# Kernel optimization log

Hardware: AMD Instinct MI355X
Metric: run time of the kernel (lower is better)

The kernel has to match this reference:

```python
import jax, jax.numpy as jnp
import numpy as np


def setup_inputs() -> dict:
    key = jax.random.key(0)
    ks = jax.random.split(key, 9)
    B, L, D, H, E = 8, 2048, 1024, 256, 8
    Hg = D // 4
    s = 0.02
    return {
        "x": jax.random.normal(ks[0], (B, L, D), dtype=jnp.float32),
        "wg1": jax.random.normal(ks[1], (D, Hg), dtype=jnp.float32) * s,
        "bg1": jax.random.normal(ks[2], (Hg,), dtype=jnp.float32) * s,
        "wg2": jax.random.normal(ks[3], (Hg, E), dtype=jnp.float32) * s,
        "bg2": jax.random.normal(ks[4], (E,), dtype=jnp.float32) * s,
        "w1": jax.random.normal(ks[5], (E, D, H), dtype=jnp.float32) * (1.0 / np.sqrt(D)),
        "b1": jax.random.normal(ks[6], (E, H), dtype=jnp.float32) * s,
        "w2": jax.random.normal(ks[7], (E, H, D), dtype=jnp.float32) * (1.0 / np.sqrt(H)),
        "b2": jax.random.normal(ks[8], (E, D), dtype=jnp.float32) * s,
        "k": 2,
    }


def reference(x, wg1, bg1, wg2, bg2, w1, b1, w2, b2, k):
    B, L, D = x.shape
    xt = x.reshape(-1, D)                       # [T, D] tokens
    T = xt.shape[0]
    # gating MLP: Linear -> GELU(exact, matches torch nn.GELU) -> Linear -> softmax
    logits = jax.nn.gelu(xt @ wg1 + bg1, approximate=False) @ wg2 + bg2  # [T, E]
    scores = jax.nn.softmax(logits, axis=-1)
    top_v, top_i = jax.lax.top_k(scores, k)     # [T, k]
    # dense gate matrix (equivalent to compute_gating's scatter); zeros for non-top-k
    gates = jnp.zeros_like(scores).at[jnp.arange(T)[:, None], top_i].set(top_v)  # [T, E]

    # grouped-GEMM MoE: y[t] = sum_e gates[t,e] * (gelu(x[t] @ W1_e + b1_e) @ W2_e + b2_e)
    # scan over the fixed, small expert axis; gates zero out non-selected experts,
    # giving math identical to the sort/dispatch + per-expert torch.mm loop.
    def body(acc, we):
        w1e, b1e, w2e, b2e, ge = we
        h = jax.nn.gelu(xt @ w1e + b1e, approximate=False)  # [T, H]
        o = h @ w2e + b2e                                    # [T, D]
        return acc + ge[:, None] * o, None

    y, _ = jax.lax.scan(body, jnp.zeros_like(xt), (w1, b1, w2, b2, gates.T))
    return y.reshape(B, L, D)
```

## Files before the change

### kernel.cpp

```cpp
#include <hip/hip_runtime.h>

typedef unsigned short u16;
typedef __attribute__((ext_vector_type(8))) short bf16x8;
typedef __attribute__((ext_vector_type(4))) float f32x4;
typedef __attribute__((ext_vector_type(4))) u16 u16x4;

#define T_TOK 16384
#define D_DIM 1024
#define NE 8
#define MAXP 33792

__device__ __forceinline__ u16 f2bf(float f) {
  union { float f; unsigned int u; } c; c.f = f;
  unsigned int u = c.u;
  u += 0x7fffu + ((u >> 16) & 1u);
  return (u16)(u >> 16);
}

__device__ __forceinline__ float bf2f(u16 v) {
  union { unsigned int u; float f; } c; c.u = ((unsigned int)v) << 16;
  return c.f;
}

__device__ __forceinline__ float gelu_exact(float u) {
  return 0.5f * u * (1.0f + erff(u * 0.70710678118654752f));
}

__device__ __forceinline__ void gld16(const void* g, void* l) {
  __builtin_amdgcn_global_load_lds(
      (const __attribute__((address_space(1))) unsigned int*)g,
      (__attribute__((address_space(3))) unsigned int*)l, 16, 0, 0);
}

__device__ __forceinline__ void stage_tile(u16* lds, const char* g0, size_t stride,
                                           int wid, int lane) {
  const char* g = g0 + (size_t)(wid * 8 + (lane >> 3)) * stride + (size_t)((lane & 7) * 16);
  char* l = (char*)lds + wid * 1024;
  #pragma unroll
  for (int c = 0; c < 4; ++c)
    gld16(g + (size_t)(32 * c) * stride, l + c * 4096);
}

__device__ __forceinline__ void stage_b32(u16* lds, const u16* mat, int rowbase,
                                          int k0, int wid, int lane) {
  const char* g0 = (const char*)(mat + (size_t)rowbase * 1024 + k0);
  #pragma unroll
  for (int c = 0; c < 2; ++c) {
    const int row = c * 64 + wid * 16 + (lane >> 2);
    const char* g = g0 + (size_t)row * 2048 + (size_t)((lane & 3) * 16);
    char* l = (char*)lds + c * 4096 + wid * 1024;
    gld16(g, l);
  }
}

__device__ __forceinline__ void mma_step(const u16* As, const u16* Bs, f32x4 acc[4][4],
                                         int wm, int wn, int lane) {
  const int r = lane & 15, kq = (lane >> 4) * 8;
  #pragma unroll
  for (int ks = 0; ks < 2; ++ks) {
    const int col = ks * 32 + kq;
    bf16x8 a[4], b[4];
    #pragma unroll
    for (int mf = 0; mf < 4; ++mf)
      a[mf] = *(const bf16x8*)&As[(wm * 64 + mf * 16 + r) * 64 + col];
    #pragma unroll
    for (int nf = 0; nf < 4; ++nf)
      b[nf] = *(const bf16x8*)&Bs[(wn * 64 + nf * 16 + r) * 64 + col];
    #pragma unroll
    for (int mf = 0; mf < 4; ++mf)
      #pragma unroll
      for (int nf = 0; nf < 4; ++nf)
        acc[mf][nf] = __builtin_amdgcn_mfma_f32_16x16x32_bf16(a[mf], b[nf], acc[mf][nf], 0, 0, 0);
  }
}

__global__ __launch_bounds__(256) void transpose_cvt_kernel(const float* __restrict__ in,
                                                            u16* __restrict__ out,
                                                            int R, int C) {
  __shared__ u16 t[32][36];
  const int e = blockIdx.z;
  const int r0 = blockIdx.x * 32, c0 = blockIdx.y * 32;
  const int tid = threadIdx.x;
  {
    const int r = tid >> 3, cq = (tid & 7) * 4;
    float4 v = *(const float4*)(in + ((size_t)e * R + r0 + r) * C + c0 + cq);
    t[r][cq + 0] = f2bf(v.x); t[r][cq + 1] = f2bf(v.y);
    t[r][cq + 2] = f2bf(v.z); t[r][cq + 3] = f2bf(v.w);
  }
  __syncthreads();
  {
    const int c = tid >> 3, rq = (tid & 7) * 4;
    u16x4 o;
    o.x = t[rq + 0][c]; o.y = t[rq + 1][c]; o.z = t[rq + 2][c]; o.w = t[rq + 3][c];
    *(u16x4*)(out + ((size_t)e * C + c0 + c) * R + r0 + rq) = o;
  }
}

__global__ __launch_bounds__(256) void transpose_hilo_kernel(const float* __restrict__ in,
                                                             u16* __restrict__ out_hi,
                                                             u16* __restrict__ out_lo,
                                                             int R, int C) {
  __shared__ u16 th[32][36];
  __shared__ u16 tl[32][36];
  const int r0 = blockIdx.x * 32, c0 = blockIdx.y * 32;
  const int tid = threadIdx.x;
  {
    const int r = tid >> 3, cq = (tid & 7) * 4;
    float4 v = *(const float4*)(in + (size_t)(r0 + r) * C + c0 + cq);
    float vv[4] = {v.x, v.y, v.z, v.w};
    #pragma unroll
    for (int i = 0; i < 4; ++i) {
      u16 h = f2bf(vv[i]);
      th[r][cq + i] = h;
      tl[r][cq + i] = f2bf(vv[i] - bf2f(h));
    }
  }
  __syncthreads();
  {
    const int c = tid >> 3, rq = (tid & 7) * 4;
    u16x4 oh, ol;
    oh.x = th[rq + 0][c]; oh.y = th[rq + 1][c]; oh.z = th[rq + 2][c]; oh.w = th[rq + 3][c];
    ol.x = tl[rq + 0][c]; ol.y = tl[rq + 1][c]; ol.z = tl[rq + 2][c]; ol.w = tl[rq + 3][c];
    *(u16x4*)(out_hi + (size_t)(c0 + c) * R + r0 + rq) = oh;
    *(u16x4*)(out_lo + (size_t)(c0 + c) * R + r0 + rq) = ol;
  }
}

__global__ __launch_bounds__(256) void gating_mfma_kernel(
    const float* __restrict__ x, const u16* __restrict__ wg1t_hi,
    const u16* __restrict__ wg1t_lo, u16* __restrict__ xb,
    float* __restrict__ p_buf) {
  __shared__ u16 Ah[2][128 * 32], Al[2][128 * 32];
  __shared__ u16 Bh[2][128 * 32], Bl[2][128 * 32];
  const int tid = threadIdx.x, lane = tid & 63, wid = tid >> 6;
  const int t0 = blockIdx.x * 128, n0 = blockIdx.y * 128;
  const int kh = blockIdx.z, kbeg = kh * 512;
  const int wm = wid >> 1, wn = wid & 1;
  const bool emit = (blockIdx.y == 0);
  const int arow = tid >> 1, akb = (tid & 1) * 16;

  f32x4 acc[4][4];
  #pragma unroll
  for (int i = 0; i < 4; ++i)
    #pragma unroll
    for (int j = 0; j < 4; ++j) acc[i][j] = (f32x4){0.f, 0.f, 0.f, 0.f};

  stage_b32(Bh[0], wg1t_hi, n0, kbeg, wid, lane);
  stage_b32(Bl[0], wg1t_lo, n0, kbeg, wid, lane);
  {
    const float* src = x + (size_t)(t0 + arow) * 1024 + kbeg + akb;
    #pragma unroll
    for (int i = 0; i < 4; ++i) {
      float4 v = *(const float4*)(src + i * 4);
      float vv[4] = {v.x, v.y, v.z, v.w};
      u16x4 h, l;
      u16 hh[4], ll[4];
      #pragma unroll
      for (int q = 0; q < 4; ++q) { hh[q] = f2bf(vv[q]); ll[q] = f2bf(vv[q] - bf2f(hh[q])); }
      h.x = hh[0]; h.y = hh[1]; h.z = hh[2]; h.w = hh[3];
      l.x = ll[0]; l.y = ll[1]; l.z = ll[2]; l.w = ll[3];
      *(u16x4*)&Ah[0][arow * 32 + akb + i * 4] = h;
      *(u16x4*)&Al[0][arow * 32 + akb + i * 4] = l;
      if (emit) *(u16x4*)(xb + (size_t)(t0 + arow) * 1024 + kbeg + akb + i * 4) = h;
    }
  }
  __syncthreads();

  int cur = 0;
  for (int kt = 0; kt < 16; ++kt) {
    const bool has_next = kt < 15;
    const int nxt = cur ^ 1;
    float4 xv[4];
    if (has_next) {
      stage_b32(Bh[nxt], wg1t_hi, n0, kbeg + (kt + 1) * 32, wid, lane);
      stage_b32(Bl[nxt], wg1t_lo, n0, kbeg + (kt + 1) * 32, wid, lane);
      const float* src = x + (size_t)(t0 + arow) * 1024 + kbeg + (kt + 1) * 32 + akb;
      #pragma unroll
      for (int i = 0; i < 4; ++i) xv[i] = *(const float4*)(src + i * 4);
    }
    {
      const int r = lane & 15, kq = (lane >> 4) * 8;
      bf16x8 ah[4], al[4], bh[4], bl[4];
      #pragma unroll
      for (int mf = 0; mf < 4; ++mf) {
        const int ro = (wm * 64 + mf * 16 + r) * 32 + kq;
        ah[mf] = *(const bf16x8*)&Ah[cur][ro];
        al[mf] = *(const bf16x8*)&Al[cur][ro];
      }
      #pragma unroll
      for (int nf = 0; nf < 4; ++nf) {
        const int ro = (wn * 64 + nf * 16 + r) * 32 + kq;
        bh[nf] = *(const bf16x8*)&Bh[cur][ro];
        bl[nf] = *(const bf16x8*)&Bl[cur][ro];
      }
      #pragma unroll
      for (int mf = 0; mf < 4; ++mf)
        #pragma unroll
        for (int nf = 0; nf < 4; ++nf) {
          acc[mf][nf] = __builtin_amdgcn_mfma_f32_16x16x32_bf16(ah[mf], bh[nf], acc[mf][nf], 0, 0, 0);
          acc[mf][nf] = __builtin_amdgcn_mfma_f32_16x16x32_bf16(ah[mf], bl[nf], acc[mf][nf], 0, 0, 0);
          acc[mf][nf] = __builtin_amdgcn_mfma_f32_16x16x32_bf16(al[mf], bh[nf], acc[mf][nf], 0, 0, 0);
        }
    }
    if (has_next) {
      #pragma unroll
      for (int i = 0; i < 4; ++i) {
        float vv[4] = {xv[i].x, xv[i].y, xv[i].z, xv[i].w};
        u16x4 h, l;
        u16 hh[4], ll[4];
        #pragma unroll
        for (int q = 0; q < 4; ++q) { hh[q] = f2bf(vv[q]); ll[q] = f2bf(vv[q] - bf2f(hh[q])); }
        h.x = hh[0]; h.y = hh[1]; h.z = hh[2]; h.w = hh[3];
        l.x = ll[0]; l.y = ll[1]; l.z = ll[2]; l.w = ll[3];
        *(u16x4*)&Ah[nxt][arow * 32 + akb + i * 4] = h;
        *(u16x4*)&Al[nxt][arow * 32 + akb + i * 4] = l;
        if (emit)
          *(u16x4*)(xb + (size_t)(t0 + arow) * 1024 + kbeg + (kt + 1) * 32 + akb + i * 4) = h;
      }
    }
    __syncthreads();
    cur ^= 1;
  }

  #pragma unroll
  for (int mf = 0; mf < 4; ++mf)
    #pragma unroll
    for (int rr = 0; rr < 4; ++rr) {
      const int lt = wm * 64 + mf * 16 + ((lane >> 4) << 2) + rr;
      #pragma unroll
      for (int nf = 0; nf < 4; ++nf) {
        const int ln = wn * 64 + nf * 16 + (lane & 15);
        p_buf[((size_t)kh * T_TOK + t0 + lt) * 256 + n0 + ln] = acc[mf][nf][rr];
      }
    }
}

__global__ __launch_bounds__(256) void gating_p2_kernel(
    const float* __restrict__ p_buf, const float* __restrict__ bg1,
    const float* __restrict__ wg2, const float* __restrict__ bg2,
    int* __restrict__ top_i, float2* __restrict__ top_g) {
  const int tid = threadIdx.x;
  const int tn = tid & 31, tm = tid >> 5;
  const int t0 = blockIdx.x * 32;

  float bb[8];
  {
    float4 ba = *(const float4*)&bg1[tn * 4];
    float4 bc = *(const float4*)&bg1[128 + tn * 4];
    bb[0] = ba.x; bb[1] = ba.y; bb[2] = ba.z; bb[3] = ba.w;
    bb[4] = bc.x; bb[5] = bc.y; bb[6] = bc.z; bb[7] = bc.w;
  }

  float hv[4][8];
  #pragma unroll
  for (int i = 0; i < 4; ++i) {
    const size_t t = t0 + tm * 4 + i;
    const float* pa = &p_buf[t * 256];
    const float* pb = &p_buf[((size_t)T_TOK + t) * 256];
    float4 a0 = *(const float4*)&pa[tn * 4];
    float4 a1 = *(const float4*)&pa[128 + tn * 4];
    float4 b0 = *(const float4*)&pb[tn * 4];
    float4 b1 = *(const float4*)&pb[128 + tn * 4];
    hv[i][0] = gelu_exact(a0.x + b0.x + bb[0]);
    hv[i][1] = gelu_exact(a0.y + b0.y + bb[1]);
    hv[i][2] = gelu_exact(a0.z + b0.z + bb[2]);
    hv[i][3] = gelu_exact(a0.w + b0.w + bb[3]);
    hv[i][4] = gelu_exact(a1.x + b1.x + bb[4]);
    hv[i][5] = gelu_exact(a1.y + b1.y + bb[5]);
    hv[i][6] = gelu_exact(a1.z + b1.z + bb[6]);
    hv[i][7] = gelu_exact(a1.w + b1.w + bb[7]);
  }

  float part[4][8];
  #pragma unroll
  for (int i = 0; i < 4; ++i)
    #pragma unroll
    for (int e = 0; e < 8; ++e) part[i][e] = 0.f;
  #pragma unroll
  for (int j = 0; j < 8; ++j) {
    const int col = (j < 4) ? (tn * 4 + j) : (128 + tn * 4 + (j - 4));
    float4 wa = *(const float4*)&wg2[col * 8];
    float4 wb = *(const float4*)&wg2[col * 8 + 4];
    float we[8] = {wa.x, wa.y, wa.z, wa.w, wb.x, wb.y, wb.z, wb.w};
    #pragma unroll
    for (int i = 0; i < 4; ++i)
      #pragma unroll
      for (int e = 0; e < 8; ++e) part[i][e] += hv[i][j] * we[e];
  }
  #pragma unroll
  for (int mask = 1; mask < 32; mask <<= 1)
    #pragma unroll
    for (int i = 0; i < 4; ++i)
      #pragma unroll
      for (int e = 0; e < 8; ++e) part[i][e] += __shfl_xor(part[i][e], mask);

  if (tn < 4) {
    float lg[8];
    #pragma unroll
    for (int i = 0; i < 4; ++i)
      if (tn == i) {
        #pragma unroll
        for (int e = 0; e < 8; ++e) lg[e] = part[i][e];
      }
    #pragma unroll
    for (int e = 0; e < 8; ++e) lg[e] += bg2[e];
    float m = lg[0];
    #pragma unroll
    for (int e = 1; e < 8; ++e) m = fmaxf(m, lg[e]);
    float ex[8], s = 0.f;
    #pragma unroll
    for (int e = 0; e < 8; ++e) { ex[e] = expf(lg[e] - m); s += ex[e]; }
    int i1 = 0;
    #pragma unroll
    for (int e = 1; e < 8; ++e) if (lg[e] > lg[i1]) i1 = e;
    int i2 = (i1 == 0) ? 1 : 0;
    #pragma unroll
    for (int e = 0; e < 8; ++e) if (e != i1 && lg[e] > lg[i2]) i2 = e;
    float inv = 1.f / s;
    const int t = t0 + tm * 4 + tn;
    top_i[t] = i1 | (i2 << 8);
    top_g[t] = make_float2(ex[i1] * inv, ex[i2] * inv);
  }
}

__global__ __launch_bounds__(256) void hist_kernel(const int* __restrict__ top_i,
                                                   int* __restrict__ hist) {
  __shared__ int h[NE];
  const int tid = threadIdx.x;
  if (tid < NE) h[tid] = 0;
  __syncthreads();
  const int ti = top_i[blockIdx.x * 256 + tid];
  atomicAdd(&h[ti & 255], 1);
  atomicAdd(&h[ti >> 8], 1);
  __syncthreads();
  if (tid < NE) hist[blockIdx.x * NE + tid] = h[tid];
}

__global__ __launch_bounds__(64) void scan_kernel(const int* __restrict__ hist,
                                                  int* __restrict__ cnt,
                                                  int* __restrict__ offs,
                                                  int* __restrict__ cbase) {
  __shared__ int tot[NE], off_s[NE];
  const int tid = threadIdx.x;
  if (tid < NE) {
    int s = 0;
    for (int c = 0; c < 64; ++c) s += hist[c * NE + tid];
    tot[tid] = s; cnt[tid] = s;
  }
  __syncthreads();
  if (tid == 0) {
    int o = 0;
    #pragma unroll
    for (int e = 0; e < NE; ++e) { off_s[e] = o; o += (tot[e] + 127) & ~127; }
  }
  __syncthreads();
  if (tid < NE) {
    offs[tid] = off_s[tid];
    int r = off_s[tid];
    for (int c = 0; c < 64; ++c) { cbase[c * NE + tid] = r; r += hist[c * NE + tid]; }
  }
}

__global__ __launch_bounds__(256) void fill_kernel(
    const int* __restrict__ top_i, const int* __restrict__ cbase,
    int* __restrict__ tok_list, int* __restrict__ pos1, int* __restrict__ pos2) {
  __shared__ int lcnt[NE];
  const int tid = threadIdx.x;
  if (tid < NE) lcnt[tid] = 0;
  __syncthreads();
  const int t = blockIdx.x * 256 + tid;
  const int ti = top_i[t];
  const int i1 = ti & 255, i2 = ti >> 8;
  const int r1 = atomicAdd(&lcnt[i1], 1);
  const int r2 = atomicAdd(&lcnt[i2], 1);
  const int p1 = cbase[blockIdx.x * NE + i1] + r1;
  const int p2 = cbase[blockIdx.x * NE + i2] + r2;
  tok_list[p1] = t; tok_list[p2] = t;
  pos1[t] = p1; pos2[t] = p2;
}

__global__ __launch_bounds__(256) void expert_h_kernel(
    const u16* __restrict__ xb, const u16* __restrict__ w1t,
    const float* __restrict__ b1, const int* __restrict__ tok_list,
    const int* __restrict__ cnt, const int* __restrict__ offs,
    u16* __restrict__ h_c) {
  __shared__ u16 As[64 * 64];
  __shared__ u16 Bs[128 * 64];
  __shared__ float b1_s[128];
  const int e = blockIdx.z;
  const int nblk = (cnt[e] + 63) >> 6;
  if ((int)blockIdx.x >= nblk) return;
  const int tid = threadIdx.x, lane = tid & 63, wid = tid >> 6;
  const int base = offs[e] + blockIdx.x * 64;
  const int n0 = blockIdx.y * 128;
  const int wm = wid >> 1, wn = wid & 1;

  if (tid < 128) b1_s[tid] = b1[e * 256 + n0 + tid];

  int tk[2];
  #pragma unroll
  for (int c = 0; c < 2; ++c)
    tk[c] = tok_list[base + (wid * 2 + c) * 8 + (lane >> 3)];

  f32x4 acc[2][4];
  #pragma unroll
  for (int i = 0; i < 2; ++i)
    #pragma unroll
    for (int j = 0; j < 4; ++j) acc[i][j] = (f32x4){0.f, 0.f, 0.f, 0.f};

  const char* Bb = (const char*)w1t + ((size_t)e * 256 + n0) * 2048;
  const int cb = (lane & 7) * 16;
  for (int kt = 0; kt < 16; ++kt) {
    __syncthreads();
    {
      char* l = (char*)As + wid * 2048;
      #pragma unroll
      for (int c = 0; c < 2; ++c)
        gld16((const char*)xb + (size_t)tk[c] * 2048 + kt * 128 + cb, l + c * 1024);
    }
    stage_tile(Bs, Bb + kt * 128, 2048, wid, lane);
    __syncthreads();
    {
      const int r = lane & 15, kq = (lane >> 4) * 8;
      #pragma unroll
      for (int ks = 0; ks < 2; ++ks) {
        const int col = ks * 32 + kq;
        bf16x8 a[2], b[4];
        #pragma unroll
        for (int mf = 0; mf < 2; ++mf)
          a[mf] = *(const bf16x8*)&As[(wm * 32 + mf * 16 + r) * 64 + col];
        #pragma unroll
        for (int nf = 0; nf < 4; ++nf)
          b[nf] = *(const bf16x8*)&Bs[(wn * 64 + nf * 16 + r) * 64 + col];
        #pragma unroll
        for (int mf = 0; mf < 2; ++mf)
          #pragma unroll
          for (int nf = 0; nf < 4; ++nf)
            acc[mf][nf] = __builtin_amdgcn_mfma_f32_16x16x32_bf16(a[mf], b[nf], acc[mf][nf], 0, 0, 0);
      }
    }
  }

  #pragma unroll
  for (int mf = 0; mf < 2; ++mf)
    #pragma unroll
    for (int rr = 0; rr < 4; ++rr) {
      const int lt = wm * 32 + mf * 16 + ((lane >> 4) << 2) + rr;
      #pragma unroll
      for (int nf = 0; nf < 4; ++nf) {
        const int ln = wn * 64 + nf * 16 + (lane & 15);
        float u = acc[mf][nf][rr] + b1_s[ln];
        h_c[(size_t)(base + lt) * 256 + n0 + ln] = f2bf(gelu_exact(u));
      }
    }
}

__global__ __launch_bounds__(256) void moe_out_kernel(
    const u16* __restrict__ h_c, const u16* __restrict__ w2t,
    const float* __restrict__ b2, const int* __restrict__ cnt,
    const int* __restrict__ offs, u16* __restrict__ o_c) {
  __shared__ u16 As[128 * 64];
  __shared__ u16 Bs[128 * 64];
  __shared__ float b2_s[128];
  const int e = blockIdx.z;
  const int nblk = (cnt[e] + 127) >> 7;
  if ((int)blockIdx.x >= nblk) return;
  const int tid = threadIdx.x, lane = tid & 63, wid = tid >> 6;
  const int base = offs[e] + blockIdx.x * 128;
  const int n0 = blockIdx.y * 128;
  const int wm = wid >> 1, wn = wid & 1;

  if (tid < 128) b2_s[tid] = b2[(size_t)e * 1024 + n0 + tid];

  f32x4 acc[4][4];
  #pragma unroll
  for (int i = 0; i < 4; ++i)
    #pragma unroll
    for (int j = 0; j < 4; ++j) acc[i][j] = (f32x4){0.f, 0.f, 0.f, 0.f};

  const char* Ab = (const char*)h_c + (size_t)base * 512;
  const char* Bb = (const char*)w2t + ((size_t)e * D_DIM + n0) * 512;
  #pragma unroll 1
  for (int kt = 0; kt < 4; ++kt) {
    __syncthreads();
    stage_tile(As, Ab + kt * 128, 512, wid, lane);
    stage_tile(Bs, Bb + kt * 128, 512, wid, lane);
    __syncthreads();
    mma_step(As, Bs, acc, wm, wn, lane);
  }

  #pragma unroll
  for (int mf = 0; mf < 4; ++mf)
    #pragma unroll
    for (int rr = 0; rr < 4; ++rr) {
      const int lt = wm * 64 + mf * 16 + ((lane >> 4) << 2) + rr;
      #pragma unroll
      for (int nf = 0; nf < 4; ++nf) {
        const int ln = wn * 64 + nf * 16 + (lane & 15);
        o_c[(size_t)(base + lt) * 1024 + n0 + ln] = f2bf(acc[mf][nf][rr] + b2_s[ln]);
      }
    }
}

__global__ __launch_bounds__(256) void gather_kernel(
    const u16* __restrict__ o_c, const int* __restrict__ pos1,
    const int* __restrict__ pos2, const float2* __restrict__ top_g,
    float* __restrict__ y) {
  const int t = blockIdx.x;
  const int p1 = pos1[t], p2 = pos2[t];
  const float2 g = top_g[t];
  const int c = threadIdx.x * 4;
  u16x4 a = *(const u16x4*)&o_c[(size_t)p1 * 1024 + c];
  u16x4 b = *(const u16x4*)&o_c[(size_t)p2 * 1024 + c];
  float4 o;
  o.x = g.x * bf2f(a.x) + g.y * bf2f(b.x);
  o.y = g.x * bf2f(a.y) + g.y * bf2f(b.y);
  o.z = g.x * bf2f(a.z) + g.y * bf2f(b.z);
  o.w = g.x * bf2f(a.w) + g.y * bf2f(b.w);
  *(float4*)&y[(size_t)t * 1024 + c] = o;
}

extern "C" void kernel_launch(void* const* d_in, const int* in_sizes, int n_in,
                              void* d_out, int out_size, void* d_ws, size_t ws_size,
                              hipStream_t stream) {
  (void)in_sizes; (void)n_in; (void)out_size; (void)ws_size;
  const float* x   = (const float*)d_in[0];
  const float* wg1 = (const float*)d_in[1];
  const float* bg1 = (const float*)d_in[2];
  const float* wg2 = (const float*)d_in[3];
  const float* bg2 = (const float*)d_in[4];
  const float* w1  = (const float*)d_in[5];
  const float* b1  = (const float*)d_in[6];
  const float* w2  = (const float*)d_in[7];
  const float* b2  = (const float*)d_in[8];
  float* y = (float*)d_out;

  char* ws = (char*)d_ws;
  u16* xb   = (u16*)(ws);
  u16* w1t  = (u16*)(ws + 33554432);
  u16* w2t  = (u16*)(ws + 37748736);
  char* M   = ws + 41943040;
  int*    cnt      = (int*)(M);
  int*    offs     = (int*)(M + 64);
  int*    hist     = (int*)(M + 128);
  int*    cbase    = (int*)(M + 2304);
  int*    tok_list = (int*)(M + 4608);
  int*    top_i    = (int*)(M + 139776);
  float2* top_g    = (float2*)(M + 205312);
  int*    pos1     = (int*)(M + 336384);
  int*    pos2     = (int*)(M + 401920);
  u16* h_c = (u16*)(ws + 42467328);
  u16* o_c = (u16*)(ws + 59768832);
  float* p_buf   = (float*)(ws + 59768832);
  u16*   wg1t_hi = (u16*)(ws + 93323264);
  u16*   wg1t_lo = (u16*)(ws + 93847552);

  hipMemsetAsync(tok_list, 0, 135168, stream);
  transpose_cvt_kernel<<<dim3(32, 8, 8), 256, 0, stream>>>(w1, w1t, 1024, 256);
  transpose_cvt_kernel<<<dim3(8, 32, 8), 256, 0, stream>>>(w2, w2t, 256, 1024);
  transpose_hilo_kernel<<<dim3(32, 8), 256, 0, stream>>>(wg1, wg1t_hi, wg1t_lo, 1024, 256);
  gating_mfma_kernel<<<dim3(128, 2, 2), 256, 0, stream>>>(x, wg1t_hi, wg1t_lo, xb, p_buf);
  gating_p2_kernel<<<512, 256, 0, stream>>>(p_buf, bg1, wg2, bg2, top_i, top_g);
  hist_kernel<<<64, 256, 0, stream>>>(top_i, hist);
  scan_kernel<<<1, 64, 0, stream>>>(hist, cnt, offs, cbase);
  fill_kernel<<<64, 256, 0, stream>>>(top_i, cbase, tok_list, pos1, pos2);
  expert_h_kernel<<<dim3(256, 2, 8), 256, 0, stream>>>(xb, w1t, b1, tok_list, cnt, offs, h_c);
  moe_out_kernel <<<dim3(128, 8, 8), 256, 0, stream>>>(h_c, w2t, b2, cnt, offs, o_c);
  gather_kernel  <<<16384, 256, 0, stream>>>(o_c, pos1, pos2, top_g, y);
}
```

Before: 189.2 us.

## Load gating A operand straight into registers and shrink N tile to 64

The gating GEMM no longer stages the fp32 x tile through shared memory as hi/lo bf16. Each wave now loads its own 32 token rows directly into MFMA register fragments, and only the weight tile goes through LDS. The N tile per block shrinks from 128 to 64, so the grid doubles to 512 blocks and LDS use drops sharply, which should raise occupancy and remove the A-side LDS traffic. In exchange, x is read from global memory twice as many times (once per N block), and each wave does less MFMA work per LDS B load.

```diff
diff --git a/kernel.cpp b/kernel.cpp
--- a/kernel.cpp
+++ b/kernel.cpp
@@ -41,15 +41,22 @@
     gld16(g + (size_t)(32 * c) * stride, l + c * 4096);
 }
 
-__device__ __forceinline__ void stage_b32(u16* lds, const u16* mat, int rowbase,
-                                          int k0, int wid, int lane) {
-  const char* g0 = (const char*)(mat + (size_t)rowbase * 1024 + k0);
-  #pragma unroll
-  for (int c = 0; c < 2; ++c) {
-    const int row = c * 64 + wid * 16 + (lane >> 2);
-    const char* g = g0 + (size_t)row * 2048 + (size_t)((lane & 3) * 16);
-    char* l = (char*)lds + c * 4096 + wid * 1024;
-    gld16(g, l);
+__device__ __forceinline__ void stage_b64x32(u16* lds, const u16* mat, int rowbase,
+                                             int k0, int wid, int lane) {
+  const int row = wid * 16 + (lane >> 2);
+  const char* g = (const char*)(mat + (size_t)(rowbase + row) * 1024 + k0 + (lane & 3) * 8);
+  char* l = (char*)lds + wid * 1024;
+  gld16(g, l);
+}
+
+__device__ __forceinline__ void split8(const float4& u, const float4& v,
+                                       bf16x8& h, bf16x8& l) {
+  float vv[8] = {u.x, u.y, u.z, u.w, v.x, v.y, v.z, v.w};
+  #pragma unroll
+  for (int i = 0; i < 8; ++i) {
+    u16 hh = f2bf(vv[i]);
+    h[i] = (short)hh;
+    l[i] = (short)f2bf(vv[i] - bf2f(hh));
   }
 }
 
@@ -130,38 +137,33 @@
     const float* __restrict__ x, const u16* __restrict__ wg1t_hi,
     const u16* __restrict__ wg1t_lo, u16* __restrict__ xb,
     float* __restrict__ p_buf) {
-  __shared__ u16 Ah[2][128 * 32], Al[2][128 * 32];
-  __shared__ u16 Bh[2][128 * 32], Bl[2][128 * 32];
+  __shared__ u16 Bh[2][64 * 32], Bl[2][64 * 32];
   const int tid = threadIdx.x, lane = tid & 63, wid = tid >> 6;
-  const int t0 = blockIdx.x * 128, n0 = blockIdx.y * 128;
+  const int t0 = blockIdx.x * 128, n0 = blockIdx.y * 64;
   const int kh = blockIdx.z, kbeg = kh * 512;
-  const int wm = wid >> 1, wn = wid & 1;
   const bool emit = (blockIdx.y == 0);
-  const int arow = tid >> 1, akb = (tid & 1) * 16;
-
-  f32x4 acc[4][4];
-  #pragma unroll
-  for (int i = 0; i < 4; ++i)
+  const int r = lane & 15;
+  const int ko = (lane >> 4) * 8;
+  const size_t row0 = t0 + wid * 32 + r;
+  const size_t row1 = row0 + 16;
+
+  f32x4 acc[2][4];
+  #pragma unroll
+  for (int i = 0; i < 2; ++i)
     #pragma unroll
     for (int j = 0; j < 4; ++j) acc[i][j] = (f32x4){0.f, 0.f, 0.f, 0.f};
 
-  stage_b32(Bh[0], wg1t_hi, n0, kbeg, wid, lane);
-  stage_b32(Bl[0], wg1t_lo, n0, kbeg, wid, lane);
+  stage_b64x32(Bh[0], wg1t_hi, n0, kbeg, wid, lane);
+  stage_b64x32(Bl[0], wg1t_lo, n0, kbeg, wid, lane);
+  bf16x8 ah[2], al[2];
   {
-    const float* src = x + (size_t)(t0 + arow) * 1024 + kbeg + akb;
-    #pragma unroll
-    for (int i = 0; i < 4; ++i) {
-      float4 v = *(const float4*)(src + i * 4);
-      float vv[4] = {v.x, v.y, v.z, v.w};
-      u16x4 h, l;
-      u16 hh[4], ll[4];
-      #pragma unroll
-      for (int q = 0; q < 4; ++q) { hh[q] = f2bf(vv[q]); ll[q] = f2bf(vv[q] - bf2f(hh[q])); }
-      h.x = hh[0]; h.y = hh[1]; h.z = hh[2]; h.w = hh[3];
-      l.x = ll[0]; l.y = ll[1]; l.z = ll[2]; l.w = ll[3];
-      *(u16x4*)&Ah[0][arow * 32 + akb + i * 4] = h;
-      *(u16x4*)&Al[0][arow * 32 + akb + i * 4] = l;
-      if (emit) *(u16x4*)(xb + (size_t)(t0 + arow) * 1024 + kbeg + akb + i * 4) = h;
+    const float* p0 = x + row0 * 1024 + kbeg + ko;
+    const float* p1 = x + row1 * 1024 + kbeg + ko;
+    split8(*(const float4*)p0, *(const float4*)(p0 + 4), ah[0], al[0]);
+    split8(*(const float4*)p1, *(const float4*)(p1 + 4), ah[1], al[1]);
+    if (emit) {
+      *(bf16x8*)(xb + row0 * 1024 + kbeg + ko) = ah[0];
+      *(bf16x8*)(xb + row1 * 1024 + kbeg + ko) = ah[1];
     }
   }
   __syncthreads();
@@ -170,52 +172,35 @@
   for (int kt = 0; kt < 16; ++kt) {
     const bool has_next = kt < 15;
     const int nxt = cur ^ 1;
-    float4 xv[4];
+    float4 an[4];
     if (has_next) {
-      stage_b32(Bh[nxt], wg1t_hi, n0, kbeg + (kt + 1) * 32, wid, lane);
-      stage_b32(Bl[nxt], wg1t_lo, n0, kbeg + (kt + 1) * 32, wid, lane);
-      const float* src = x + (size_t)(t0 + arow) * 1024 + kbeg + (kt + 1) * 32 + akb;
-      #pragma unroll
-      for (int i = 0; i < 4; ++i) xv[i] = *(const float4*)(src + i * 4);
-    }
-    {
-      const int r = lane & 15, kq = (lane >> 4) * 8;
-      bf16x8 ah[4], al[4], bh[4], bl[4];
-      #pragma unroll
-      for (int mf = 0; mf < 4; ++mf) {
-        const int ro = (wm * 64 + mf * 16 + r) * 32 + kq;
-        ah[mf] = *(const bf16x8*)&Ah[cur][ro];
-        al[mf] = *(const bf16x8*)&Al[cur][ro];
-      }
-      #pragma unroll
-      for (int nf = 0; nf < 4; ++nf) {
-        const int ro = (wn * 64 + nf * 16 + r) * 32 + kq;
-        bh[nf] = *(const bf16x8*)&Bh[cur][ro];
-        bl[nf] = *(const bf16x8*)&Bl[cur][ro];
-      }
-      #pragma unroll
-      for (int mf = 0; mf < 4; ++mf)
-        #pragma unroll
-        for (int nf = 0; nf < 4; ++nf) {
-          acc[mf][nf] = __builtin_amdgcn_mfma_f32_16x16x32_bf16(ah[mf], bh[nf], acc[mf][nf], 0, 0, 0);
-          acc[mf][nf] = __builtin_amdgcn_mfma_f32_16x16x32_bf16(ah[mf], bl[nf], acc[mf][nf], 0, 0, 0);
-          acc[mf][nf] = __builtin_amdgcn_mfma_f32_16x16x32_bf16(al[mf], bh[nf], acc[mf][nf], 0, 0, 0);
-        }
+      const int kk = kbeg + (kt + 1) * 32;
+      stage_b64x32(Bh[nxt], wg1t_hi, n0, kk, wid, lane);
+      stage_b64x32(Bl[nxt], wg1t_lo, n0, kk, wid, lane);
+      const float* p0 = x + row0 * 1024 + kk + ko;
+      const float* p1 = x + row1 * 1024 + kk + ko;
+      an[0] = *(const float4*)p0; an[1] = *(const float4*)(p0 + 4);
+      an[2] = *(const float4*)p1; an[3] = *(const float4*)(p1 + 4);
+    }
+    #pragma unroll
+    for (int nf = 0; nf < 4; ++nf) {
+      const int ro = (nf * 16 + r) * 32 + ko;
+      bf16x8 bh = *(const bf16x8*)&Bh[cur][ro];
+      bf16x8 bl = *(const bf16x8*)&Bl[cur][ro];
+      acc[0][nf] = __builtin_amdgcn_mfma_f32_16x16x32_bf16(ah[0], bh, acc[0][nf], 0, 0, 0);
+      acc[0][nf] = __builtin_amdgcn_mfma_f32_16x16x32_bf16(ah[0], bl, acc[0][nf], 0, 0, 0);
+      acc[0][nf] = __builtin_amdgcn_mfma_f32_16x16x32_bf16(al[0], bh, acc[0][nf], 0, 0, 0);
+      acc[1][nf] = __builtin_amdgcn_mfma_f32_16x16x32_bf16(ah[1], bh, acc[1][nf], 0, 0, 0);
+      acc[1][nf] = __builtin_amdgcn_mfma_f32_16x16x32_bf16(ah[1], bl, acc[1][nf], 0, 0, 0);
+      acc[1][nf] = __builtin_amdgcn_mfma_f32_16x16x32_bf16(al[1], bh, acc[1][nf], 0, 0, 0);
     }
     if (has_next) {
-      #pragma unroll
-      for (int i = 0; i < 4; ++i) {
-        float vv[4] = {xv[i].x, xv[i].y, xv[i].z, xv[i].w};
-        u16x4 h, l;
-        u16 hh[4], ll[4];
-        #pragma unroll
-        for (int q = 0; q < 4; ++q) { hh[q] = f2bf(vv[q]); ll[q] = f2bf(vv[q] - bf2f(hh[q])); }
-        h.x = hh[0]; h.y = hh[1]; h.z = hh[2]; h.w = hh[3];
-        l.x = ll[0]; l.y = ll[1]; l.z = ll[2]; l.w = ll[3];
-        *(u16x4*)&Ah[nxt][arow * 32 + akb + i * 4] = h;
-        *(u16x4*)&Al[nxt][arow * 32 + akb + i * 4] = l;
-        if (emit)
-          *(u16x4*)(xb + (size_t)(t0 + arow) * 1024 + kbeg + (kt + 1) * 32 + akb + i * 4) = h;
+      split8(an[0], an[1], ah[0], al[0]);
+      split8(an[2], an[3], ah[1], al[1]);
+      if (emit) {
+        const int kk = kbeg + (kt + 1) * 32;
+        *(bf16x8*)(xb + row0 * 1024 + kk + ko) = ah[0];
+        *(bf16x8*)(xb + row1 * 1024 + kk + ko) = ah[1];
       }
     }
     __syncthreads();
@@ -223,13 +208,13 @@
   }
 
   #pragma unroll
-  for (int mf = 0; mf < 4; ++mf)
+  for (int mf = 0; mf < 2; ++mf)
     #pragma unroll
     for (int rr = 0; rr < 4; ++rr) {
-      const int lt = wm * 64 + mf * 16 + ((lane >> 4) << 2) + rr;
+      const int lt = wid * 32 + mf * 16 + ((lane >> 4) << 2) + rr;
       #pragma unroll
       for (int nf = 0; nf < 4; ++nf) {
-        const int ln = wn * 64 + nf * 16 + (lane & 15);
+        const int ln = nf * 16 + (lane & 15);
         p_buf[((size_t)kh * T_TOK + t0 + lt) * 256 + n0 + ln] = acc[mf][nf][rr];
       }
     }
@@ -559,7 +544,7 @@
   transpose_cvt_kernel<<<dim3(32, 8, 8), 256, 0, stream>>>(w1, w1t, 1024, 256);
   transpose_cvt_kernel<<<dim3(8, 32, 8), 256, 0, stream>>>(w2, w2t, 256, 1024);
   transpose_hilo_kernel<<<dim3(32, 8), 256, 0, stream>>>(wg1, wg1t_hi, wg1t_lo, 1024, 256);
-  gating_mfma_kernel<<<dim3(128, 2, 2), 256, 0, stream>>>(x, wg1t_hi, wg1t_lo, xb, p_buf);
+  gating_mfma_kernel<<<dim3(128, 4, 2), 256, 0, stream>>>(x, wg1t_hi, wg1t_lo, xb, p_buf);
   gating_p2_kernel<<<512, 256, 0, stream>>>(p_buf, bg1, wg2, bg2, top_i, top_g);
   hist_kernel<<<64, 256, 0, stream>>>(top_i, hist);
   scan_kernel<<<1, 64, 0, stream>>>(hist, cnt, offs, cbase);
```

Result: slower. 196.1 us (+3.7%).

## Precompute hi/lo bf16 split of x and shrink gating GEMM tile

Applied to the files above, without the earlier changes.

Adds a separate kernel that converts x once into hi and lo bf16 arrays. The gating GEMM then stages both through direct global-to-LDS loads instead of converting fp32 inline. The GEMM tile drops from 128 to 64 tokens with a single LDS buffer, doubling the grid and using fewer accumulator registers for higher occupancy. In exchange there is an extra pass over x (read fp32, write two bf16 arrays), the x tile is read twice from memory, and the software double-buffering with its compute/load overlap is removed.

```diff
diff --git a/kernel.cpp b/kernel.cpp
--- a/kernel.cpp
+++ b/kernel.cpp
@@ -41,6 +41,14 @@
     gld16(g + (size_t)(32 * c) * stride, l + c * 4096);
 }
 
+__device__ __forceinline__ void stage_b64x32(u16* lds, const u16* mat, int rowbase,
+                                             int k0, int wid, int lane) {
+  const int row = wid * 16 + (lane >> 2);
+  const char* g = (const char*)(mat + (size_t)(rowbase + row) * 1024 + k0 + (lane & 3) * 8);
+  char* l = (char*)lds + wid * 1024;
+  gld16(g, l);
+}
+
 __device__ __forceinline__ void stage_b32(u16* lds, const u16* mat, int rowbase,
                                           int k0, int wid, int lane) {
   const char* g0 = (const char*)(mat + (size_t)rowbase * 1024 + k0);
@@ -72,6 +80,22 @@
       for (int nf = 0; nf < 4; ++nf)
         acc[mf][nf] = __builtin_amdgcn_mfma_f32_16x16x32_bf16(a[mf], b[nf], acc[mf][nf], 0, 0, 0);
   }
+}
+
+__global__ __launch_bounds__(256) void cvt_hilo_x_kernel(const float* __restrict__ x,
+                                                         u16* __restrict__ xh,
+                                                         u16* __restrict__ xl) {
+  const int i = (blockIdx.x * 256 + threadIdx.x) * 4;
+  float4 v = *(const float4*)(x + i);
+  float vv[4] = {v.x, v.y, v.z, v.w};
+  u16x4 h, l;
+  u16 hh[4], ll[4];
+  #pragma unroll
+  for (int q = 0; q < 4; ++q) { hh[q] = f2bf(vv[q]); ll[q] = f2bf(vv[q] - bf2f(hh[q])); }
+  h.x = hh[0]; h.y = hh[1]; h.z = hh[2]; h.w = hh[3];
+  l.x = ll[0]; l.y = ll[1]; l.z = ll[2]; l.w = ll[3];
+  *(u16x4*)(xh + i) = h;
+  *(u16x4*)(xl + i) = l;
 }
 
 __global__ __launch_bounds__(256) void transpose_cvt_kernel(const float* __restrict__ in,
@@ -127,106 +151,57 @@
 }
 
 __global__ __launch_bounds__(256) void gating_mfma_kernel(
-    const float* __restrict__ x, const u16* __restrict__ wg1t_hi,
-    const u16* __restrict__ wg1t_lo, u16* __restrict__ xb,
+    const u16* __restrict__ xh, const u16* __restrict__ xl,
+    const u16* __restrict__ wg1t_hi, const u16* __restrict__ wg1t_lo,
     float* __restrict__ p_buf) {
-  __shared__ u16 Ah[2][128 * 32], Al[2][128 * 32];
-  __shared__ u16 Bh[2][128 * 32], Bl[2][128 * 32];
+  __shared__ u16 Ah[64 * 32], Al[64 * 32];
+  __shared__ u16 Bh[128 * 32], Bl[128 * 32];
   const int tid = threadIdx.x, lane = tid & 63, wid = tid >> 6;
-  const int t0 = blockIdx.x * 128, n0 = blockIdx.y * 128;
+  const int t0 = blockIdx.x * 64, n0 = blockIdx.y * 128;
   const int kh = blockIdx.z, kbeg = kh * 512;
   const int wm = wid >> 1, wn = wid & 1;
-  const bool emit = (blockIdx.y == 0);
-  const int arow = tid >> 1, akb = (tid & 1) * 16;
-
-  f32x4 acc[4][4];
-  #pragma unroll
-  for (int i = 0; i < 4; ++i)
+
+  f32x4 acc[2][4];
+  #pragma unroll
+  for (int i = 0; i < 2; ++i)
     #pragma unroll
     for (int j = 0; j < 4; ++j) acc[i][j] = (f32x4){0.f, 0.f, 0.f, 0.f};
 
-  stage_b32(Bh[0], wg1t_hi, n0, kbeg, wid, lane);
-  stage_b32(Bl[0], wg1t_lo, n0, kbeg, wid, lane);
-  {
-    const float* src = x + (size_t)(t0 + arow) * 1024 + kbeg + akb;
-    #pragma unroll
-    for (int i = 0; i < 4; ++i) {
-      float4 v = *(const float4*)(src + i * 4);
-      float vv[4] = {v.x, v.y, v.z, v.w};
-      u16x4 h, l;
-      u16 hh[4], ll[4];
-      #pragma unroll
-      for (int q = 0; q < 4; ++q) { hh[q] = f2bf(vv[q]); ll[q] = f2bf(vv[q] - bf2f(hh[q])); }
-      h.x = hh[0]; h.y = hh[1]; h.z = hh[2]; h.w = hh[3];
-      l.x = ll[0]; l.y = ll[1]; l.z = ll[2]; l.w = ll[3];
-      *(u16x4*)&Ah[0][arow * 32 + akb + i * 4] = h;
-      *(u16x4*)&Al[0][arow * 32 + akb + i * 4] = l;
-      if (emit) *(u16x4*)(xb + (size_t)(t0 + arow) * 1024 + kbeg + akb + i * 4) = h;
-    }
-  }
-  __syncthreads();
-
-  int cur = 0;
   for (int kt = 0; kt < 16; ++kt) {
-    const bool has_next = kt < 15;
-    const int nxt = cur ^ 1;
-    float4 xv[4];
-    if (has_next) {
-      stage_b32(Bh[nxt], wg1t_hi, n0, kbeg + (kt + 1) * 32, wid, lane);
-      stage_b32(Bl[nxt], wg1t_lo, n0, kbeg + (kt + 1) * 32, wid, lane);
-      const float* src = x + (size_t)(t0 + arow) * 1024 + kbeg + (kt + 1) * 32 + akb;
-      #pragma unroll
-      for (int i = 0; i < 4; ++i) xv[i] = *(const float4*)(src + i * 4);
-    }
-    {
-      const int r = lane & 15, kq = (lane >> 4) * 8;
-      bf16x8 ah[4], al[4], bh[4], bl[4];
-      #pragma unroll
-      for (int mf = 0; mf < 4; ++mf) {
-        const int ro = (wm * 64 + mf * 16 + r) * 32 + kq;
-        ah[mf] = *(const bf16x8*)&Ah[cur][ro];
-        al[mf] = *(const bf16x8*)&Al[cur][ro];
+    const int k0 = kbeg + kt * 32;
+    __syncthreads();
+    stage_b64x32(Ah, xh, t0, k0, wid, lane);
+    stage_b64x32(Al, xl, t0, k0, wid, lane);
+    stage_b32(Bh, wg1t_hi, n0, k0, wid, lane);
+    stage_b32(Bl, wg1t_lo, n0, k0, wid, lane);
+    __syncthreads();
+    const int r = lane & 15, ko = (lane >> 4) * 8;
+    bf16x8 ah[2], al[2];
+    #pragma unroll
+    for (int mf = 0; mf < 2; ++mf) {
+      const int ro = (wm * 32 + mf * 16 + r) * 32 + ko;
+      ah[mf] = *(const bf16x8*)&Ah[ro];
+      al[mf] = *(const bf16x8*)&Al[ro];
+    }
+    #pragma unroll
+    for (int nf = 0; nf < 4; ++nf) {
+      const int ro = (wn * 64 + nf * 16 + r) * 32 + ko;
+      bf16x8 bh = *(const bf16x8*)&Bh[ro];
+      bf16x8 bl = *(const bf16x8*)&Bl[ro];
+      #pragma unroll
+      for (int mf = 0; mf < 2; ++mf) {
+        acc[mf][nf] = __builtin_amdgcn_mfma_f32_16x16x32_bf16(ah[mf], bh, acc[mf][nf], 0, 0, 0);
+        acc[mf][nf] = __builtin_amdgcn_mfma_f32_16x16x32_bf16(ah[mf], bl, acc[mf][nf], 0, 0, 0);
+        acc[mf][nf] = __builtin_amdgcn_mfma_f32_16x16x32_bf16(al[mf], bh, acc[mf][nf], 0, 0, 0);
       }
-      #pragma unroll
-      for (int nf = 0; nf < 4; ++nf) {
-        const int ro = (wn * 64 + nf * 16 + r) * 32 + kq;
-        bh[nf] = *(const bf16x8*)&Bh[cur][ro];
-        bl[nf] = *(const bf16x8*)&Bl[cur][ro];
-      }
-      #pragma unroll
-      for (int mf = 0; mf < 4; ++mf)
-        #pragma unroll
-        for (int nf = 0; nf < 4; ++nf) {
-          acc[mf][nf] = __builtin_amdgcn_mfma_f32_16x16x32_bf16(ah[mf], bh[nf], acc[mf][nf], 0, 0, 0);
-          acc[mf][nf] = __builtin_amdgcn_mfma_f32_16x16x32_bf16(ah[mf], bl[nf], acc[mf][nf], 0, 0, 0);
-          acc[mf][nf] = __builtin_amdgcn_mfma_f32_16x16x32_bf16(al[mf], bh[nf], acc[mf][nf], 0, 0, 0);
-        }
-    }
-    if (has_next) {
-      #pragma unroll
-      for (int i = 0; i < 4; ++i) {
-        float vv[4] = {xv[i].x, xv[i].y, xv[i].z, xv[i].w};
-        u16x4 h, l;
-        u16 hh[4], ll[4];
-        #pragma unroll
-        for (int q = 0; q < 4; ++q) { hh[q] = f2bf(vv[q]); ll[q] = f2bf(vv[q] - bf2f(hh[q])); }
-        h.x = hh[0]; h.y = hh[1]; h.z = hh[2]; h.w = hh[3];
-        l.x = ll[0]; l.y = ll[1]; l.z = ll[2]; l.w = ll[3];
-        *(u16x4*)&Ah[nxt][arow * 32 + akb + i * 4] = h;
-        *(u16x4*)&Al[nxt][arow * 32 + akb + i * 4] = l;
-        if (emit)
-          *(u16x4*)(xb + (size_t)(t0 + arow) * 1024 + kbeg + (kt + 1) * 32 + akb + i * 4) = h;
-      }
-    }
-    __syncthreads();
-    cur ^= 1;
-  }
-
-  #pragma unroll
-  for (int mf = 0; mf < 4; ++mf)
+    }
+  }
+
+  #pragma unroll
+  for (int mf = 0; mf < 2; ++mf)
     #pragma unroll
     for (int rr = 0; rr < 4; ++rr) {
-      const int lt = wm * 64 + mf * 16 + ((lane >> 4) << 2) + rr;
+      const int lt = wm * 32 + mf * 16 + ((lane >> 4) << 2) + rr;
       #pragma unroll
       for (int nf = 0; nf < 4; ++nf) {
         const int ln = wn * 64 + nf * 16 + (lane & 15);
@@ -554,12 +529,14 @@
   float* p_buf   = (float*)(ws + 59768832);
   u16*   wg1t_hi = (u16*)(ws + 93323264);
   u16*   wg1t_lo = (u16*)(ws + 93847552);
+  u16*   xl      = (u16*)(ws + 94371840);
 
   hipMemsetAsync(tok_list, 0, 135168, stream);
+  cvt_hilo_x_kernel<<<16384, 256, 0, stream>>>(x, xb, xl);
   transpose_cvt_kernel<<<dim3(32, 8, 8), 256, 0, stream>>>(w1, w1t, 1024, 256);
   transpose_cvt_kernel<<<dim3(8, 32, 8), 256, 0, stream>>>(w2, w2t, 256, 1024);
   transpose_hilo_kernel<<<dim3(32, 8), 256, 0, stream>>>(wg1, wg1t_hi, wg1t_lo, 1024, 256);
-  gating_mfma_kernel<<<dim3(128, 2, 2), 256, 0, stream>>>(x, wg1t_hi, wg1t_lo, xb, p_buf);
+  gating_mfma_kernel<<<dim3(256, 2, 2), 256, 0, stream>>>(xb, xl, wg1t_hi, wg1t_lo, p_buf);
   gating_p2_kernel<<<512, 256, 0, stream>>>(p_buf, bg1, wg2, bg2, top_i, top_g);
   hist_kernel<<<64, 256, 0, stream>>>(top_i, hist);
   scan_kernel<<<1, 64, 0, stream>>>(hist, cnt, offs, cbase);
```

New measurement: 204.2 us. 7.9% more time.
